# Kernel optimization log

Hardware: AMD Instinct MI355X
Metric: run time of the kernel (lower is better)

## Reference

```python
import jax, jax.numpy as jnp
import numpy as np

INF = 1e9  # large additive-mask constant (original code's INF)
D_KEY = 64


def setup_inputs() -> dict:
    key = jax.random.key(0)
    kq, kk, kv = jax.random.split(key, 3)
    B, S, D = 8, 2048, 64
    return {
        "query": jax.random.normal(kq, (B, S, D), dtype=jnp.float32),
        "key": jax.random.normal(kk, (B, S, D), dtype=jnp.float32),
        "value": jax.random.normal(kv, (B, S, D), dtype=jnp.float32),
    }


def reference(query, key, value):
    # scores: [B, Sq, Sk]
    scores = jnp.einsum("bqd,bkd->bqk", query, key)
    Sk = key.shape[1]
    # strict upper-triangular additive causal mask, subtracted BEFORE scaling
    tri = jnp.triu(jnp.ones((Sk, Sk), dtype=scores.dtype), k=1) * INF
    scores = scores - tri[None, :, :]
    scale = jnp.asarray(np.sqrt(D_KEY), dtype=scores.dtype)
    attn = jax.nn.softmax(scores / scale, axis=2)  # dropout ratio = 0.0
    return jnp.einsum("bqk,bkd->bqd", attn, value)
```

## Files before the change

### kernel.cpp

```cpp
#include <hip/hip_runtime.h>
#include <hip/hip_bf16.h>

typedef __attribute__((ext_vector_type(8))) short bf16x8;
typedef __attribute__((ext_vector_type(4))) float f32x4;
typedef __attribute__((ext_vector_type(4))) unsigned short us4;

#define BATCH 8
#define SEQ 2048
#define DIM 64
#define QB 64
#define NQT 32
#define NKT 32
#define TE 4096
#define CH 8
#define CPB 80
#define QSCALE (0.125f * 1.44269504088896f)
#define THR 8.0f

__device__ __forceinline__ unsigned short f2bf(float f) {
    return __builtin_bit_cast(unsigned short, __float2bfloat16(f));
}

__device__ __forceinline__ int kswz(int row, int d) {
    return (row * DIM + d) ^ ((row & 7) << 3);
}
__device__ __forceinline__ int vswz(int d, int kv) {
    return (d * 64 + kv) ^ ((((d & 7) ^ ((d >> 2) & 7)) & 7) << 3);
}
__device__ __forceinline__ int pswz128(int row, int kv) {
    return (row * 128 + kv) ^ ((row & 7) << 3);
}
__device__ __forceinline__ int chunk_prefix(int qi) {
    return (qi < 8) ? qi
         : (qi < 16) ? 8 + 2 * (qi - 8)
         : (qi < 24) ? 24 + 3 * (qi - 16)
                     : 48 + 4 * (qi - 24);
}

#define GLOAD16(gsrc, ldst)                                                     \
    __builtin_amdgcn_global_load_lds(                                           \
        (const __attribute__((address_space(1))) void*)(gsrc),                  \
        (__attribute__((address_space(3))) void*)(ldst), 16, 0, 0)

#define FENCE_BARRIER_LGKM()                                   \
    do {                                                       \
        __builtin_amdgcn_sched_barrier(0);                     \
        asm volatile("s_waitcnt lgkmcnt(0)" ::: "memory");     \
        __builtin_amdgcn_s_barrier();                          \
        __builtin_amdgcn_sched_barrier(0);                     \
    } while (0)

#define FENCE_BARRIER_ALL()                                            \
    do {                                                               \
        __builtin_amdgcn_sched_barrier(0);                             \
        asm volatile("s_waitcnt vmcnt(0) lgkmcnt(0)" ::: "memory");    \
        __builtin_amdgcn_s_barrier();                                  \
        __builtin_amdgcn_sched_barrier(0);                             \
    } while (0)

__global__ __launch_bounds__(256) void prep_kernel(const float* __restrict__ K,
                                                   const float* __restrict__ V,
                                                   unsigned short* __restrict__ Kp,
                                                   unsigned short* __restrict__ Vp) {
    const int tile = blockIdx.x;
    const int tid = threadIdx.x;
    const float* Kt = K + (size_t)tile * TE;
    const float* Vt = V + (size_t)tile * TE;
    unsigned short* Kd = Kp + (size_t)tile * TE;
    unsigned short* Vd = Vp + (size_t)tile * TE;
    #pragma unroll
    for (int i = 0; i < 4; ++i) {
        int idx = i * 256 + tid;
        int row = idx >> 4;
        int d0 = (idx & 15) << 2;
        f32x4 kf = *(const f32x4*)(Kt + row * DIM + d0);
        us4 kb = {f2bf(kf[0]), f2bf(kf[1]), f2bf(kf[2]), f2bf(kf[3])};
        *(us4*)(&Kd[kswz(row, d0)]) = kb;
    }
    const int dt4 = tid & 15, k4 = tid >> 4;
    f32x4 vf[4];
    #pragma unroll
    for (int rr = 0; rr < 4; ++rr)
        vf[rr] = *(const f32x4*)(Vt + (k4 * 4 + rr) * DIM + dt4 * 4);
    #pragma unroll
    for (int dd = 0; dd < 4; ++dd) {
        us4 vb = {f2bf(vf[0][dd]), f2bf(vf[1][dd]), f2bf(vf[2][dd]), f2bf(vf[3][dd])};
        *(us4*)(&Vd[vswz(dt4 * 4 + dd, k4 * 4)]) = vb;
    }
}

__global__ __launch_bounds__(256) void fa_kernel(const float* __restrict__ Q,
                                                 const unsigned short* __restrict__ Kp,
                                                 const unsigned short* __restrict__ Vp,
                                                 float* __restrict__ PO,
                                                 float* __restrict__ PM,
                                                 float* __restrict__ PL,
                                                 float* __restrict__ O) {
    __shared__ unsigned short KL[2][8192];
    __shared__ unsigned short VL[2][8192];

    const int tid = threadIdx.x;
    const int w = tid >> 6, lane = tid & 63, g = lane >> 4, c = lane & 15;

    const int slot = blockIdx.x;
    const int batch = slot & 7;
    const int c0 = (CPB - 1) - (slot >> 3);
    int qi, sp;
    if (c0 < 8)        { qi = c0; sp = 0; }
    else if (c0 < 24)  { int x = c0 - 8;  qi = 8 + (x >> 1); sp = x & 1; }
    else if (c0 < 48)  { int x = c0 - 24; int q = x / 3; qi = 16 + q; sp = x - 3 * q; }
    else               { int x = c0 - 48; qi = 24 + (x >> 2); sp = x & 3; }

    const int q0 = qi * QB;
    const int nt = qi + 1;
    const int t0 = sp * CH;
    const int t1 = (t0 + CH < nt) ? (t0 + CH) : nt;
    const int tiles = t1 - t0;
    const int nu = (tiles + 1) >> 1;
    const bool dchunk = (t1 == nt);

    const unsigned short* Kb = Kp + (size_t)batch * NKT * TE;
    const unsigned short* Vb = Vp + (size_t)batch * NKT * TE;

    {
        int tA = t0;
        bool two0 = (t0 + 1 < t1);
        const char* Ks = (const char*)(Kb + (size_t)tA * TE);
        const char* Vs = (const char*)(Vb + (size_t)tA * TE);
        char* kd = (char*)&KL[0][0];
        char* vd = (char*)&VL[0][0];
        if (two0) {
            #pragma unroll
            for (int i = 0; i < 4; ++i) {
                int off = (w * 4 + i) * 1024;
                GLOAD16(Ks + off + lane * 16, kd + off);
                GLOAD16(Vs + off + lane * 16, vd + off);
            }
        } else {
            #pragma unroll
            for (int i = 0; i < 2; ++i) {
                int off = (w * 2 + i) * 1024;
                GLOAD16(Ks + off + lane * 16, kd + off);
                GLOAD16(Vs + off + lane * 16, vd + off);
            }
        }
    }

    const float* Qrow = Q + (size_t)(batch * SEQ + q0 + w * 16 + c) * DIM;
    f32x4 qf0 = *(const f32x4*)(Qrow + g * 8);
    f32x4 qf1 = *(const f32x4*)(Qrow + g * 8 + 4);
    f32x4 qf2 = *(const f32x4*)(Qrow + 32 + g * 8);
    f32x4 qf3 = *(const f32x4*)(Qrow + 32 + g * 8 + 4);
    bf16x8 qa[2];
    #pragma unroll
    for (int j = 0; j < 4; ++j) {
        qa[0][j]     = (short)f2bf(qf0[j] * QSCALE);
        qa[0][j + 4] = (short)f2bf(qf1[j] * QSCALE);
        qa[1][j]     = (short)f2bf(qf2[j] * QSCALE);
        qa[1][j + 4] = (short)f2bf(qf3[j] * QSCALE);
    }

    float m[4], l[4];
    f32x4 o[4];
    #pragma unroll
    for (int r = 0; r < 4; ++r) { m[r] = -1e30f; l[r] = 0.f; }
    #pragma unroll
    for (int dt = 0; dt < 4; ++dt) o[dt] = f32x4{0.f, 0.f, 0.f, 0.f};

    FENCE_BARRIER_ALL();

    for (int u = 0; u < nu; ++u) {
        const int cb = u & 1;
        const bool last = (u == nu - 1);
        const bool single = last && (tiles & 1);
        const bool dmask = last && dchunk;

        if (!last) {
            int tA = t0 + 2 * (u + 1);
            bool two = (tA + 1 < t1);
            const char* Ks = (const char*)(Kb + (size_t)tA * TE);
            const char* Vs = (const char*)(Vb + (size_t)tA * TE);
            char* kd = (char*)&KL[cb ^ 1][0];
            char* vd = (char*)&VL[cb ^ 1][0];
            if (two) {
                #pragma unroll
                for (int i = 0; i < 4; ++i) {
                    int off = (w * 4 + i) * 1024;
                    GLOAD16(Ks + off + lane * 16, kd + off);
                    GLOAD16(Vs + off + lane * 16, vd + off);
                }
            } else {
                #pragma unroll
                for (int i = 0; i < 2; ++i) {
                    int off = (w * 2 + i) * 1024;
                    GLOAD16(Ks + off + lane * 16, kd + off);
                    GLOAD16(Vs + off + lane * 16, vd + off);
                }
            }
        }

        f32x4 s[8];
        #pragma unroll
        for (int n = 0; n < 8; ++n) s[n] = f32x4{0.f, 0.f, 0.f, 0.f};
        __builtin_amdgcn_s_setprio(1);
        #pragma unroll
        for (int n = 0; n < 4; ++n)
            #pragma unroll
            for (int f = 0; f < 2; ++f) {
                int row = n * 16 + c;
                bf16x8 kb = *(bf16x8*)(&KL[cb][kswz(row, f * 32 + g * 8)]);
                s[n] = __builtin_amdgcn_mfma_f32_16x16x32_bf16(qa[f], kb, s[n], 0, 0, 0);
            }
        if (!single) {
            #pragma unroll
            for (int n = 0; n < 4; ++n)
                #pragma unroll
                for (int f = 0; f < 2; ++f) {
                    int row = (n + 4) * 16 + c;
                    bf16x8 kb = *(bf16x8*)(&KL[cb][kswz(row, f * 32 + g * 8)]);
                    s[n + 4] = __builtin_amdgcn_mfma_f32_16x16x32_bf16(qa[f], kb, s[n + 4], 0, 0, 0);
                }
        }
        __builtin_amdgcn_s_setprio(0);
        if (single) {
            #pragma unroll
            for (int n = 4; n < 8; ++n) s[n] = f32x4{-1e30f, -1e30f, -1e30f, -1e30f};
        }
        if (dmask) {
            const int dbase = (t1 - 1) * 64;
            if (single) {
                #pragma unroll
                for (int n = 0; n < 4; ++n) {
                    int col = dbase + n * 16 + c;
                    #pragma unroll
                    for (int r = 0; r < 4; ++r)
                        if (col > q0 + w * 16 + g * 4 + r) s[n][r] = -1e30f;
                }
            } else {
                #pragma unroll
                for (int n = 0; n < 4; ++n) {
                    int col = dbase + n * 16 + c;
                    #pragma unroll
                    for (int r = 0; r < 4; ++r)
                        if (col > q0 + w * 16 + g * 4 + r) s[n + 4][r] = -1e30f;
                }
            }
        }

        FENCE_BARRIER_LGKM();

        float pmax[4];
        #pragma unroll
        for (int r = 0; r < 4; ++r) {
            float t2 = fmaxf(fmaxf(fmaxf(s[0][r], s[1][r]), fmaxf(s[2][r], s[3][r])),
                             fmaxf(fmaxf(s[4][r], s[5][r]), fmaxf(s[6][r], s[7][r])));
            t2 = fmaxf(t2, __shfl_xor(t2, 1));
            t2 = fmaxf(t2, __shfl_xor(t2, 2));
            t2 = fmaxf(t2, __shfl_xor(t2, 4));
            t2 = fmaxf(t2, __shfl_xor(t2, 8));
            pmax[r] = t2;
        }
        bool need = false;
        #pragma unroll
        for (int r = 0; r < 4; ++r) need |= (pmax[r] > m[r] + THR);
        if (__any(need)) {
            #pragma unroll
            for (int r = 0; r < 4; ++r) {
                float mn = fmaxf(m[r], pmax[r]);
                float alpha = exp2f(m[r] - mn);
                m[r] = mn;
                l[r] *= alpha;
                #pragma unroll
                for (int dt = 0; dt < 4; ++dt) o[dt][r] *= alpha;
            }
        }
        float tsum[4] = {0.f, 0.f, 0.f, 0.f};
        #pragma unroll
        for (int n = 0; n < 8; ++n)
            #pragma unroll
            for (int r = 0; r < 4; ++r) {
                float pe = exp2f(s[n][r] - m[r]);
                s[n][r] = pe;
                tsum[r] += pe;
            }
        #pragma unroll
        for (int r = 0; r < 4; ++r) {
            float ts = tsum[r];
            ts += __shfl_xor(ts, 1);
            ts += __shfl_xor(ts, 2);
            ts += __shfl_xor(ts, 4);
            ts += __shfl_xor(ts, 8);
            l[r] += ts;
        }

        unsigned short* Pw = &KL[cb][w * 2048];
        #pragma unroll
        for (int n = 0; n < 8; ++n)
            #pragma unroll
            for (int r = 0; r < 4; ++r)
                Pw[pswz128(g * 4 + r, n * 16 + c)] = f2bf(s[n][r]);
        asm volatile("s_waitcnt lgkmcnt(0)" ::: "memory");
        __builtin_amdgcn_sched_barrier(0);

        __builtin_amdgcn_s_setprio(1);
        #pragma unroll
        for (int ks = 0; ks < 2; ++ks) {
            bf16x8 pa = *(bf16x8*)(&Pw[pswz128(c, ks * 32 + g * 8)]);
            #pragma unroll
            for (int dt = 0; dt < 4; ++dt) {
                int d = dt * 16 + c;
                bf16x8 vb = *(bf16x8*)(&VL[cb][vswz(d, ks * 32 + g * 8)]);
                o[dt] = __builtin_amdgcn_mfma_f32_16x16x32_bf16(pa, vb, o[dt], 0, 0, 0);
            }
        }
        if (!single) {
            #pragma unroll
            for (int ks = 0; ks < 2; ++ks) {
                bf16x8 pa = *(bf16x8*)(&Pw[pswz128(c, 64 + ks * 32 + g * 8)]);
                #pragma unroll
                for (int dt = 0; dt < 4; ++dt) {
                    int d = dt * 16 + c;
                    bf16x8 vb = *(bf16x8*)(&VL[cb][4096 + vswz(d, ks * 32 + g * 8)]);
                    o[dt] = __builtin_amdgcn_mfma_f32_16x16x32_bf16(pa, vb, o[dt], 0, 0, 0);
                }
            }
        }
        __builtin_amdgcn_s_setprio(0);

        if (!last) FENCE_BARRIER_ALL();
    }

    if (nt <= CH) {
        #pragma unroll
        for (int r = 0; r < 4; ++r) {
            float inv = 1.f / l[r];
            float* Orow = O + (size_t)(batch * SEQ + q0 + w * 16 + g * 4 + r) * DIM;
            #pragma unroll
            for (int dt = 0; dt < 4; ++dt)
                Orow[dt * 16 + c] = o[dt][r] * inv;
        }
    } else {
        float* Pbase = PO + (size_t)slot * (QB * DIM);
        #pragma unroll
        for (int r = 0; r < 4; ++r) {
            int rowin = w * 16 + g * 4 + r;
            #pragma unroll
            for (int dt = 0; dt < 4; ++dt)
                Pbase[rowin * DIM + dt * 16 + c] = o[dt][r];
            if (c == 0) {
                PM[(size_t)slot * QB + rowin] = m[r];
                PL[(size_t)slot * QB + rowin] = l[r];
            }
        }
    }
}

__global__ __launch_bounds__(256) void combine_kernel(const float* __restrict__ PO,
                                                      const float* __restrict__ PM,
                                                      const float* __restrict__ PL,
                                                      float* __restrict__ O) {
    const int tid = threadIdx.x;
    const int ridx = blockIdx.x * 16 + (tid >> 4);
    const int d0 = (tid & 15) << 2;
    const int batch = ridx / 1536;
    const int rem = ridx - batch * 1536;
    const int qi = 8 + (rem >> 6);
    const int rowin = rem & 63;
    const int nc = (qi + CH) >> 3;
    const int pfx = chunk_prefix(qi);

    float mstar = -1e30f;
    #pragma unroll 4
    for (int sp = 0; sp < nc; ++sp) {
        int slot = ((CPB - 1 - (pfx + sp)) << 3) | batch;
        mstar = fmaxf(mstar, PM[(size_t)slot * QB + rowin]);
    }
    float ls = 0.f;
    f32x4 os = {0.f, 0.f, 0.f, 0.f};
    #pragma unroll 4
    for (int sp = 0; sp < nc; ++sp) {
        int slot = ((CPB - 1 - (pfx + sp)) << 3) | batch;
        float wgt = exp2f(PM[(size_t)slot * QB + rowin] - mstar);
        ls += PL[(size_t)slot * QB + rowin] * wgt;
        f32x4 po = *(const f32x4*)(PO + (size_t)slot * (QB * DIM) + rowin * DIM + d0);
        os += po * wgt;
    }
    const int grow = batch * SEQ + qi * 64 + rowin;
    float inv = 1.f / ls;
    f32x4 res = os * inv;
    *(f32x4*)(O + (size_t)grow * DIM + d0) = res;
}

extern "C" void kernel_launch(void* const* d_in, const int* in_sizes, int n_in,
                              void* d_out, int out_size, void* d_ws, size_t ws_size,
                              hipStream_t stream) {
    const float* Q = (const float*)d_in[0];
    const float* K = (const float*)d_in[1];
    const float* V = (const float*)d_in[2];
    float* O = (float*)d_out;
    (void)in_sizes; (void)n_in; (void)out_size; (void)ws_size;

    const size_t kvelems = (size_t)BATCH * SEQ * DIM;
    unsigned short* Kp = (unsigned short*)d_ws;
    unsigned short* Vp = Kp + kvelems;
    float* PO = (float*)(Vp + kvelems);
    float* PM = PO + (size_t)BATCH * CPB * QB * DIM;
    float* PL = PM + (size_t)BATCH * CPB * QB;

    prep_kernel<<<BATCH * NKT, 256, 0, stream>>>(K, V, Kp, Vp);
    fa_kernel<<<BATCH * CPB, 256, 0, stream>>>(Q, Kp, Vp, PO, PM, PL, O);
    combine_kernel<<<BATCH * 24 * 64 / 16, 256, 0, stream>>>(PO, PM, PL, O);
}
```

Baseline: 45.03 us.

## Process one 64-key tile per iteration with separate P buffer and higher occupancy

The flash-attention loop now processes one 64-key tile per iteration instead of pairs of tiles. This halves the K/V LDS double buffers and gives each wave its own P staging buffer, so P no longer overwrites the K buffer. That removes the mid-iteration LDS barrier, and launch_bounds(256,4) asks for four blocks per CU to hide latency. The prep kernel's block-to-tile mapping is also interleaved across batches. The cost is twice as many loop iterations and barriers per block, and fewer MFMAs between global-load waits.

```diff
diff --git a/kernel.cpp b/kernel.cpp
--- a/kernel.cpp
+++ b/kernel.cpp
@@ -27,8 +27,8 @@
 __device__ __forceinline__ int vswz(int d, int kv) {
     return (d * 64 + kv) ^ ((((d & 7) ^ ((d >> 2) & 7)) & 7) << 3);
 }
-__device__ __forceinline__ int pswz128(int row, int kv) {
-    return (row * 128 + kv) ^ ((row & 7) << 3);
+__device__ __forceinline__ int pswz(int row, int kv) {
+    return (row * 64 + kv) ^ ((row & 7) << 3);
 }
 __device__ __forceinline__ int chunk_prefix(int qi) {
     return (qi < 8) ? qi
@@ -42,27 +42,13 @@
         (const __attribute__((address_space(1))) void*)(gsrc),                  \
         (__attribute__((address_space(3))) void*)(ldst), 16, 0, 0)
 
-#define FENCE_BARRIER_LGKM()                                   \
-    do {                                                       \
-        __builtin_amdgcn_sched_barrier(0);                     \
-        asm volatile("s_waitcnt lgkmcnt(0)" ::: "memory");     \
-        __builtin_amdgcn_s_barrier();                          \
-        __builtin_amdgcn_sched_barrier(0);                     \
-    } while (0)
-
-#define FENCE_BARRIER_ALL()                                            \
-    do {                                                               \
-        __builtin_amdgcn_sched_barrier(0);                             \
-        asm volatile("s_waitcnt vmcnt(0) lgkmcnt(0)" ::: "memory");    \
-        __builtin_amdgcn_s_barrier();                                  \
-        __builtin_amdgcn_sched_barrier(0);                             \
-    } while (0)
-
 __global__ __launch_bounds__(256) void prep_kernel(const float* __restrict__ K,
                                                    const float* __restrict__ V,
                                                    unsigned short* __restrict__ Kp,
                                                    unsigned short* __restrict__ Vp) {
-    const int tile = blockIdx.x;
+    const int batch = blockIdx.x & 7;
+    const int t = blockIdx.x >> 3;
+    const int tile = batch * NKT + t;
     const int tid = threadIdx.x;
     const float* Kt = K + (size_t)tile * TE;
     const float* Vt = V + (size_t)tile * TE;
@@ -89,15 +75,16 @@
     }
 }
 
-__global__ __launch_bounds__(256) void fa_kernel(const float* __restrict__ Q,
-                                                 const unsigned short* __restrict__ Kp,
-                                                 const unsigned short* __restrict__ Vp,
-                                                 float* __restrict__ PO,
-                                                 float* __restrict__ PM,
-                                                 float* __restrict__ PL,
-                                                 float* __restrict__ O) {
-    __shared__ unsigned short KL[2][8192];
-    __shared__ unsigned short VL[2][8192];
+__global__ __launch_bounds__(256, 4) void fa_kernel(const float* __restrict__ Q,
+                                                    const unsigned short* __restrict__ Kp,
+                                                    const unsigned short* __restrict__ Vp,
+                                                    float* __restrict__ PO,
+                                                    float* __restrict__ PM,
+                                                    float* __restrict__ PL,
+                                                    float* __restrict__ O) {
+    __shared__ unsigned short KL[2][4096];
+    __shared__ unsigned short VL[2][4096];
+    __shared__ unsigned short PB[4][1024];
 
     const int tid = threadIdx.x;
     const int w = tid >> 6, lane = tid & 63, g = lane >> 4, c = lane & 15;
@@ -116,35 +103,26 @@
     const int t0 = sp * CH;
     const int t1 = (t0 + CH < nt) ? (t0 + CH) : nt;
     const int tiles = t1 - t0;
-    const int nu = (tiles + 1) >> 1;
     const bool dchunk = (t1 == nt);
 
     const unsigned short* Kb = Kp + (size_t)batch * NKT * TE;
     const unsigned short* Vb = Vp + (size_t)batch * NKT * TE;
 
-    {
-        int tA = t0;
-        bool two0 = (t0 + 1 < t1);
-        const char* Ks = (const char*)(Kb + (size_t)tA * TE);
-        const char* Vs = (const char*)(Vb + (size_t)tA * TE);
-        char* kd = (char*)&KL[0][0];
-        char* vd = (char*)&VL[0][0];
-        if (two0) {
-            #pragma unroll
-            for (int i = 0; i < 4; ++i) {
-                int off = (w * 4 + i) * 1024;
-                GLOAD16(Ks + off + lane * 16, kd + off);
-                GLOAD16(Vs + off + lane * 16, vd + off);
-            }
-        } else {
-            #pragma unroll
-            for (int i = 0; i < 2; ++i) {
-                int off = (w * 2 + i) * 1024;
-                GLOAD16(Ks + off + lane * 16, kd + off);
-                GLOAD16(Vs + off + lane * 16, vd + off);
-            }
-        }
-    }
+#define STAGE_TILE(tidx, buf)                                          \
+    do {                                                               \
+        const char* Ks_ = (const char*)(Kb + (size_t)(tidx) * TE);     \
+        const char* Vs_ = (const char*)(Vb + (size_t)(tidx) * TE);     \
+        char* kd_ = (char*)&KL[buf][0];                                \
+        char* vd_ = (char*)&VL[buf][0];                                \
+        _Pragma("unroll")                                              \
+        for (int i_ = 0; i_ < 2; ++i_) {                               \
+            int off_ = (w * 2 + i_) * 1024;                            \
+            GLOAD16(Ks_ + off_ + lane * 16, kd_ + off_);               \
+            GLOAD16(Vs_ + off_ + lane * 16, vd_ + off_);               \
+        }                                                              \
+    } while (0)
+
+    STAGE_TILE(t0, 0);
 
     const float* Qrow = Q + (size_t)(batch * SEQ + q0 + w * 16 + c) * DIM;
     f32x4 qf0 = *(const f32x4*)(Qrow + g * 8);
@@ -167,93 +145,45 @@
     #pragma unroll
     for (int dt = 0; dt < 4; ++dt) o[dt] = f32x4{0.f, 0.f, 0.f, 0.f};
 
-    FENCE_BARRIER_ALL();
-
-    for (int u = 0; u < nu; ++u) {
+    __builtin_amdgcn_sched_barrier(0);
+    asm volatile("s_waitcnt vmcnt(0)" ::: "memory");
+    __builtin_amdgcn_s_barrier();
+    __builtin_amdgcn_sched_barrier(0);
+
+    for (int u = 0; u < tiles; ++u) {
         const int cb = u & 1;
-        const bool last = (u == nu - 1);
-        const bool single = last && (tiles & 1);
-        const bool dmask = last && dchunk;
-
-        if (!last) {
-            int tA = t0 + 2 * (u + 1);
-            bool two = (tA + 1 < t1);
-            const char* Ks = (const char*)(Kb + (size_t)tA * TE);
-            const char* Vs = (const char*)(Vb + (size_t)tA * TE);
-            char* kd = (char*)&KL[cb ^ 1][0];
-            char* vd = (char*)&VL[cb ^ 1][0];
-            if (two) {
+        const bool last = (u == tiles - 1);
+
+        if (!last) STAGE_TILE(t0 + u + 1, cb ^ 1);
+
+        f32x4 s[4];
+        #pragma unroll
+        for (int n = 0; n < 4; ++n) s[n] = f32x4{0.f, 0.f, 0.f, 0.f};
+        __builtin_amdgcn_s_setprio(1);
+        #pragma unroll
+        for (int n = 0; n < 4; ++n)
+            #pragma unroll
+            for (int f = 0; f < 2; ++f) {
+                bf16x8 kb = *(bf16x8*)(&KL[cb][kswz(n * 16 + c, f * 32 + g * 8)]);
+                s[n] = __builtin_amdgcn_mfma_f32_16x16x32_bf16(qa[f], kb, s[n], 0, 0, 0);
+            }
+        __builtin_amdgcn_s_setprio(0);
+
+        if (dchunk && last) {
+            const int dbase = (nt - 1) * 64;
+            #pragma unroll
+            for (int n = 0; n < 4; ++n) {
+                int col = dbase + n * 16 + c;
                 #pragma unroll
-                for (int i = 0; i < 4; ++i) {
-                    int off = (w * 4 + i) * 1024;
-                    GLOAD16(Ks + off + lane * 16, kd + off);
-                    GLOAD16(Vs + off + lane * 16, vd + off);
-                }
-            } else {
-                #pragma unroll
-                for (int i = 0; i < 2; ++i) {
-                    int off = (w * 2 + i) * 1024;
-                    GLOAD16(Ks + off + lane * 16, kd + off);
-                    GLOAD16(Vs + off + lane * 16, vd + off);
-                }
-            }
-        }
-
-        f32x4 s[8];
-        #pragma unroll
-        for (int n = 0; n < 8; ++n) s[n] = f32x4{0.f, 0.f, 0.f, 0.f};
-        __builtin_amdgcn_s_setprio(1);
-        #pragma unroll
-        for (int n = 0; n < 4; ++n)
-            #pragma unroll
-            for (int f = 0; f < 2; ++f) {
-                int row = n * 16 + c;
-                bf16x8 kb = *(bf16x8*)(&KL[cb][kswz(row, f * 32 + g * 8)]);
-                s[n] = __builtin_amdgcn_mfma_f32_16x16x32_bf16(qa[f], kb, s[n], 0, 0, 0);
-            }
-        if (!single) {
-            #pragma unroll
-            for (int n = 0; n < 4; ++n)
-                #pragma unroll
-                for (int f = 0; f < 2; ++f) {
-                    int row = (n + 4) * 16 + c;
-                    bf16x8 kb = *(bf16x8*)(&KL[cb][kswz(row, f * 32 + g * 8)]);
-                    s[n + 4] = __builtin_amdgcn_mfma_f32_16x16x32_bf16(qa[f], kb, s[n + 4], 0, 0, 0);
-                }
-        }
-        __builtin_amdgcn_s_setprio(0);
-        if (single) {
-            #pragma unroll
-            for (int n = 4; n < 8; ++n) s[n] = f32x4{-1e30f, -1e30f, -1e30f, -1e30f};
-        }
-        if (dmask) {
-            const int dbase = (t1 - 1) * 64;
-            if (single) {
-                #pragma unroll
-                for (int n = 0; n < 4; ++n) {
-                    int col = dbase + n * 16 + c;
-                    #pragma unroll
-                    for (int r = 0; r < 4; ++r)
-                        if (col > q0 + w * 16 + g * 4 + r) s[n][r] = -1e30f;
-                }
-            } else {
-                #pragma unroll
-                for (int n = 0; n < 4; ++n) {
-                    int col = dbase + n * 16 + c;
-                    #pragma unroll
-                    for (int r = 0; r < 4; ++r)
-                        if (col > q0 + w * 16 + g * 4 + r) s[n + 4][r] = -1e30f;
-                }
-            }
-        }
-
-        FENCE_BARRIER_LGKM();
+                for (int r = 0; r < 4; ++r)
+                    if (col > q0 + w * 16 + g * 4 + r) s[n][r] = -1e30f;
+            }
+        }
 
         float pmax[4];
         #pragma unroll
         for (int r = 0; r < 4; ++r) {
-            float t2 = fmaxf(fmaxf(fmaxf(s[0][r], s[1][r]), fmaxf(s[2][r], s[3][r])),
-                             fmaxf(fmaxf(s[4][r], s[5][r]), fmaxf(s[6][r], s[7][r])));
+            float t2 = fmaxf(fmaxf(s[0][r], s[1][r]), fmaxf(s[2][r], s[3][r]));
             t2 = fmaxf(t2, __shfl_xor(t2, 1));
             t2 = fmaxf(t2, __shfl_xor(t2, 2));
             t2 = fmaxf(t2, __shfl_xor(t2, 4));
@@ -276,7 +206,7 @@
         }
         float tsum[4] = {0.f, 0.f, 0.f, 0.f};
         #pragma unroll
-        for (int n = 0; n < 8; ++n)
+        for (int n = 0; n < 4; ++n)
             #pragma unroll
             for (int r = 0; r < 4; ++r) {
                 float pe = exp2f(s[n][r] - m[r]);
@@ -293,41 +223,33 @@
             l[r] += ts;
         }
 
-        unsigned short* Pw = &KL[cb][w * 2048];
-        #pragma unroll
-        for (int n = 0; n < 8; ++n)
+        unsigned short* Pw = &PB[w][0];
+        #pragma unroll
+        for (int n = 0; n < 4; ++n)
             #pragma unroll
             for (int r = 0; r < 4; ++r)
-                Pw[pswz128(g * 4 + r, n * 16 + c)] = f2bf(s[n][r]);
+                Pw[pswz(g * 4 + r, n * 16 + c)] = f2bf(s[n][r]);
         asm volatile("s_waitcnt lgkmcnt(0)" ::: "memory");
         __builtin_amdgcn_sched_barrier(0);
 
         __builtin_amdgcn_s_setprio(1);
         #pragma unroll
         for (int ks = 0; ks < 2; ++ks) {
-            bf16x8 pa = *(bf16x8*)(&Pw[pswz128(c, ks * 32 + g * 8)]);
+            bf16x8 pa = *(bf16x8*)(&Pw[pswz(c, ks * 32 + g * 8)]);
             #pragma unroll
             for (int dt = 0; dt < 4; ++dt) {
-                int d = dt * 16 + c;
-                bf16x8 vb = *(bf16x8*)(&VL[cb][vswz(d, ks * 32 + g * 8)]);
+                bf16x8 vb = *(bf16x8*)(&VL[cb][vswz(dt * 16 + c, ks * 32 + g * 8)]);
                 o[dt] = __builtin_amdgcn_mfma_f32_16x16x32_bf16(pa, vb, o[dt], 0, 0, 0);
             }
         }
-        if (!single) {
-            #pragma unroll
-            for (int ks = 0; ks < 2; ++ks) {
-                bf16x8 pa = *(bf16x8*)(&Pw[pswz128(c, 64 + ks * 32 + g * 8)]);
-                #pragma unroll
-                for (int dt = 0; dt < 4; ++dt) {
-                    int d = dt * 16 + c;
-                    bf16x8 vb = *(bf16x8*)(&VL[cb][4096 + vswz(d, ks * 32 + g * 8)]);
-                    o[dt] = __builtin_amdgcn_mfma_f32_16x16x32_bf16(pa, vb, o[dt], 0, 0, 0);
-                }
-            }
-        }
         __builtin_amdgcn_s_setprio(0);
 
-        if (!last) FENCE_BARRIER_ALL();
+        if (!last) {
+            __builtin_amdgcn_sched_barrier(0);
+            asm volatile("s_waitcnt vmcnt(0)" ::: "memory");
+            __builtin_amdgcn_s_barrier();
+            __builtin_amdgcn_sched_barrier(0);
+        }
     }
 
     if (nt <= CH) {
@@ -353,6 +275,7 @@
             }
         }
     }
+#undef STAGE_TILE
 }
 
 __global__ __launch_bounds__(256) void combine_kernel(const float* __restrict__ PO,
```

Measured after the change: 42.03 us. 6.7% less time.
